# Kernel optimization log

Measured on AMD Instinct MI355X. Metric: run time of the kernel, lower is better.

The kernel has to match this reference:

```python
import jax, jax.numpy as jnp
import numpy as np
import math

V, L, D, S, F, H, B = 32000, 6, 1024, 2048, 4096, 16, 2
DK = D // H
EPS = 1e-5


def _pos_encoding(max_len, d_model):
    pos = np.arange(max_len)[:, None].astype(np.float32)
    freq = np.exp(np.arange(0, d_model, 2).astype(np.float32) * -(math.log(10000.0) / d_model))
    pe = np.zeros((max_len, d_model), dtype=np.float32)
    pe[:, 0::2] = np.sin(pos * freq)
    pe[:, 1::2] = np.cos(pos * freq)
    return jnp.asarray(pe)


def setup_inputs() -> dict:
    key = jax.random.key(0)
    ks = jax.random.split(key, 16)
    n = lambda k, shape: (jax.random.normal(k, shape, dtype=jnp.float32) * 0.02)
    return {
        "tokens": jax.random.randint(ks[0], (B, S), 0, V, dtype=jnp.int32),
        "emb": n(ks[1], (V, D)),
        "Wq": n(ks[2], (L, D, D)), "bq": jnp.zeros((L, D)),
        "Wk": n(ks[3], (L, D, D)), "bk": jnp.zeros((L, D)),
        "Wv": n(ks[4], (L, D, D)), "bv": jnp.zeros((L, D)),
        "Wo": n(ks[5], (L, D, D)), "bo": jnp.zeros((L, D)),
        "W1": n(ks[6], (L, D, F)), "b1": jnp.zeros((L, F)),
        "W2": n(ks[7], (L, F, D)), "b2": jnp.zeros((L, D)),
        "g1": jnp.ones((L, D)), "be1": jnp.zeros((L, D)),
        "g2": jnp.ones((L, D)), "be2": jnp.zeros((L, D)),
    }


def _layernorm(x, g, b):
    mu = jnp.mean(x, axis=-1, keepdims=True)
    var = jnp.var(x, axis=-1, keepdims=True)
    return (x - mu) * jax.lax.rsqrt(var + EPS) * g + b


def _encoder(tokens, emb, Wq, bq, Wk, bk, Wv, bv, Wo, bo, W1, b1, W2, b2, g1, be1, g2, be2):
    pe = _pos_encoding(S, D)
    x = emb[tokens] * jnp.float32(math.sqrt(D)) + pe  # [B,S,D]

    def layer(x, p):
        wq, bq_, wk, bk_, wv, bv_, wo, bo_, w1, b1_, w2, b2_, g1_, be1_, g2_, be2_ = p
        q = (x @ wq + bq_).reshape(B, S, H, DK)
        k = (x @ wk + bk_).reshape(B, S, H, DK)
        v = (x @ wv + bv_).reshape(B, S, H, DK)
        scores = jnp.einsum("bqhd,bkhd->bhqk", q, k) / jnp.float32(math.sqrt(DK))
        attn = jax.nn.softmax(scores, axis=-1)
        out = jnp.einsum("bhqk,bkhd->bqhd", attn, v).reshape(B, S, D)
        out = out @ wo + bo_
        x = _layernorm(x + out, g1_, be1_)
        ff = jax.nn.relu(x @ w1 + b1_) @ w2 + b2_
        x = _layernorm(x + ff, g2_, be2_)
        return x, None

    params = (Wq, bq, Wk, bk, Wv, bv, Wo, bo, W1, b1, W2, b2, g1, be1, g2, be2)
    x, _ = jax.lax.scan(layer, x, params)
    return x


def reference(tokens, emb, Wq, bq, Wk, bk, Wv, bv, Wo, bo, W1, b1, W2, b2, g1, be1, g2, be2):
    return _encoder(tokens, emb, Wq, bq, Wk, bk, Wv, bv, Wo, bo, W1, b1, W2, b2, g1, be1, g2, be2)
```

## Files before the change

kernel.cpp:

```cpp
#include <hip/hip_runtime.h>
#include <hip/hip_bf16.h>

#define DEV static __device__ __forceinline__

typedef __attribute__((ext_vector_type(8))) short bf16x8;
typedef __attribute__((ext_vector_type(4))) float f32x4;
typedef __attribute__((ext_vector_type(4))) unsigned short u16x4;
typedef __attribute__((ext_vector_type(4))) unsigned int u32x4;

constexpr int Lc = 6, Dc = 1024, Sc = 2048, Fc = 4096, Hc = 16, Bc = 2;
constexpr int Mc = Bc * Sc;
constexpr int QKVN = 3 * Dc;
constexpr float QSCALE = 0.18033688011112042f;

DEV float bf2f(unsigned short u) {
  unsigned int x = ((unsigned int)u) << 16; float f;
  __builtin_memcpy(&f, &x, 4); return f;
}
DEV unsigned short f2bf(float f) {
  unsigned int x; __builtin_memcpy(&x, &f, 4);
  x += 0x7fffu + ((x >> 16) & 1u);
  return (unsigned short)(x >> 16);
}
DEV unsigned int cvt_pk_bf16(float lo, float hi) {
  unsigned int r;
  asm("v_cvt_pk_bf16_f32 %0, %1, %2" : "=v"(r) : "v"(lo), "v"(hi));
  return r;
}

typedef __attribute__((address_space(1))) unsigned int* gas_t;
typedef __attribute__((address_space(3))) unsigned int* las_t;
DEV void gload16(const void* g, void* l) {
  __builtin_amdgcn_global_load_lds((gas_t)g, (las_t)l, 16, 0, 0);
}

DEV int vperm(int k) {
  return ((k >> 5) << 5) + (((k >> 2) & 3) << 3) + (((k >> 4) & 1) << 2) + (k & 3);
}

DEV void tr32(const float* __restrict__ W, unsigned short* __restrict__ Wt,
              int Kd, int Nd, float scale, int bx, int by, int tid,
              float (*tile)[33])
{
  const int n0 = bx * 32, k0 = by * 32;
  const int tx = tid & 31, ty = tid >> 5;
#pragma unroll
  for (int i = 0; i < 4; ++i) {
    int k = ty + i * 8;
    tile[k][tx] = W[(size_t)(k0 + k) * Nd + n0 + tx];
  }
  __syncthreads();
#pragma unroll
  for (int i = 0; i < 4; ++i) {
    int n = ty + i * 8;
    Wt[(size_t)(n0 + n) * Kd + k0 + tx] = f2bf(tile[tx][n] * scale);
  }
}

__global__ __launch_bounds__(256) void prep_weights(
    const float* __restrict__ Wq, const float* __restrict__ Wk,
    const float* __restrict__ Wv, const float* __restrict__ Wo,
    const float* __restrict__ W1, const float* __restrict__ W2,
    const float* __restrict__ bq, const float* __restrict__ bk,
    const float* __restrict__ bv,
    unsigned short* __restrict__ Wqkvt, unsigned short* __restrict__ Wot,
    unsigned short* __restrict__ W1t, unsigned short* __restrict__ W2t,
    float* __restrict__ bqkv)
{
  __shared__ float tile[32][33];
  const int id = blockIdx.x, t = threadIdx.x;
  if (id < 4096) {
    int which = id >> 10, lo = id & 1023;
    int bx = lo & 31, by = lo >> 5;
    if (which == 0)      tr32(Wq, Wqkvt, Dc, Dc, QSCALE, bx, by, t, tile);
    else if (which == 1) tr32(Wk, Wqkvt + (size_t)Dc * Dc, Dc, Dc, 1.0f, bx, by, t, tile);
    else if (which == 2) tr32(Wv, Wqkvt + (size_t)2 * Dc * Dc, Dc, Dc, 1.0f, bx, by, t, tile);
    else                 tr32(Wo, Wot, Dc, Dc, 1.0f, bx, by, t, tile);
  } else if (id < 8192) {
    int lo = id - 4096;
    tr32(W1, W1t, Dc, Fc, 1.0f, lo & 127, lo >> 7, t, tile);
  } else if (id < 12288) {
    int lo = id - 8192;
    tr32(W2, W2t, Fc, Dc, 1.0f, lo & 31, lo >> 5, t, tile);
  } else {
    int i = (id - 12288) * 256 + t;
    bqkv[i] = (i < Dc) ? bq[i] * QSCALE : (i < 2 * Dc ? bk[i - Dc] : bv[i - 2 * Dc]);
  }
}

__global__ __launch_bounds__(256) void embed_kernel(
    const int* __restrict__ tokens, const float* __restrict__ emb,
    float* __restrict__ xf, unsigned short* __restrict__ xb)
{
  const int bs = blockIdx.x;
  const int s = bs & (Sc - 1);
  const int tok = tokens[bs];
  const int d0 = threadIdx.x * 4;
  f32x4 e4 = *(const f32x4*)(emb + (size_t)tok * Dc + d0);
  f32x4 vf; u16x4 vb;
#pragma unroll
  for (int j = 0; j < 4; ++j) {
    int d = d0 + j;
    float e = e4[j] * 32.0f;
    float fr = expf((float)(d & ~1) * (-9.210340371976184f / 1024.0f));
    float arg = (float)s * fr;
    float pe = (d & 1) ? cosf(arg) : sinf(arg);
    float v = e + pe;
    vf[j] = v; vb[j] = f2bf(v);
  }
  *(f32x4*)(xf + (size_t)bs * Dc + d0) = vf;
  *(u16x4*)(xb + (size_t)bs * Dc + d0) = vb;
}

DEV void gemm256_core(const unsigned short* __restrict__ A,
                      const unsigned short* __restrict__ Bt,
                      unsigned short (*As)[256 * 64], unsigned short (*Bs)[256 * 64],
                      f32x4 (*acc)[4], int mTile, int nTile,
                      int Kstride, int k0, int nT, int t)
{
  const int lane = t & 63;
  const int g = lane >> 4, li = lane & 15;
  const int w = t >> 6;
  const int wm = w >> 2, wn = w & 3;
  const int trow = t >> 3, tslot = t & 7;
  const int asl = tslot ^ (trow & 7);
  int aoff[4];
#pragma unroll
  for (int q = 0; q < 4; ++q) {
    int R = (trow < 32) ? (q * 32 + trow) : (96 + q * 32 + trow);
    aoff[q] = (mTile + R) * Kstride + k0 + asl * 8;
  }
  int boff[4], bld[4];
#pragma unroll
  for (int k2 = 0; k2 < 4; ++k2) {
    int idx = k2 * 512 + t;
    int br = idx >> 3;
    int bs = (idx & 7) ^ (br & 7);
    boff[k2] = (nTile + br) * Kstride + k0 + bs * 8;
    bld[k2] = idx * 8;
  }

  auto stB = [&](int nb, int kt, int ph) {
    gload16(Bt + boff[ph * 2 + 0] + kt, &Bs[nb][bld[ph * 2 + 0]]);
    gload16(Bt + boff[ph * 2 + 1] + kt, &Bs[nb][bld[ph * 2 + 1]]);
  };
  auto stA = [&](int nb, int kt, int ph) {
    gload16(A + aoff[ph * 2 + 0] + kt, &As[nb][(ph * 2 + 0) * 4096 + t * 8]);
    gload16(A + aoff[ph * 2 + 1] + kt, &As[nb][(ph * 2 + 1) * 4096 + t * 8]);
  };

  stB(0, 0, 0); stB(0, 0, 1); stA(0, 0, 0); stA(0, 0, 1);
  asm volatile("s_waitcnt vmcnt(0)" ::: "memory");
  __builtin_amdgcn_s_barrier();

  int cur = 0;
  for (int tt = 0; tt < nT; ++tt) {
    const char* Ac = (const char*)As[cur];
    const char* Bc = (const char*)Bs[cur];
    const int nb = cur ^ 1;
    const int ktn = (tt + 1) << 6;
    const bool more = tt + 1 < nT;

    bf16x8 bfr[4][2];
#pragma unroll
    for (int ni = 0; ni < 4; ++ni) {
      const int rn = wn * 64 + ni * 16 + li;
#pragma unroll
      for (int ks = 0; ks < 2; ++ks) {
        const int kb = ks * 64 + (g << 4);
        bfr[ni][ks] = *(const bf16x8*)(Bc + rn * 128 + (kb ^ ((rn & 7) << 4)));
      }
    }

#pragma unroll
    for (int ph = 0; ph < 4; ++ph) {
      bf16x8 afr[2][2];
#pragma unroll
      for (int mi2 = 0; mi2 < 2; ++mi2) {
        const int rr = wm * 32 + mi2 * 16 + li;
#pragma unroll
        for (int ks = 0; ks < 2; ++ks) {
          const int kb = ks * 64 + (g << 4);
          afr[mi2][ks] = *(const bf16x8*)(Ac + ph * 8192 + rr * 128 + (kb ^ ((rr & 7) << 4)));
        }
      }
      if (more) {
        if (ph == 0)      stB(nb, ktn, 0);
        else if (ph == 1) stB(nb, ktn, 1);
        else if (ph == 2) stA(nb, ktn, 0);
        else              stA(nb, ktn, 1);
      }
      __builtin_amdgcn_s_barrier();
      __builtin_amdgcn_s_setprio(1);
#pragma unroll
      for (int mi2 = 0; mi2 < 2; ++mi2)
#pragma unroll
        for (int ni = 0; ni < 4; ++ni)
#pragma unroll
          for (int ks = 0; ks < 2; ++ks)
            acc[ph * 2 + mi2][ni] = __builtin_amdgcn_mfma_f32_16x16x32_bf16(
                afr[mi2][ks], bfr[ni][ks], acc[ph * 2 + mi2][ni], 0, 0, 0);
      __builtin_amdgcn_s_setprio(0);
      if (ph == 0)      asm volatile("s_waitcnt vmcnt(4)" ::: "memory");
      else if (ph == 1) asm volatile("s_waitcnt vmcnt(5)" ::: "memory");
      else if (ph == 2) asm volatile("s_waitcnt vmcnt(6)" ::: "memory");
      else              asm volatile("s_waitcnt vmcnt(3)" ::: "memory");
      __builtin_amdgcn_s_barrier();
    }
    cur ^= 1;
  }
}

__global__ __launch_bounds__(512) void gemm256(
    const unsigned short* __restrict__ A, const unsigned short* __restrict__ Bt,
    const float* __restrict__ bias, unsigned short* __restrict__ outB,
    unsigned short* __restrict__ Vt, int gx, int Ndim, int Kdim, int relu)
{
  __shared__ alignas(16) unsigned short As[2][256 * 64];
  __shared__ alignas(16) unsigned short Bs[2][256 * 64];
  const int t = threadIdx.x;
  const int lane = t & 63, w = t >> 6;
  const int wm = w >> 2, wn = w & 3;
  const int g = lane >> 4, li = lane & 15;
  const int nwg = gridDim.x, flat = blockIdx.x;
  const int swz = (flat & 7) * (nwg >> 3) + (flat >> 3);
  const int mTile = (swz / gx) * 256;
  const int nTile = (swz % gx) * 256;

  f32x4 acc[8][4] = {};
  gemm256_core(A, Bt, As, Bs, acc, mTile, nTile, Kdim, 0, Kdim >> 6, t);

  const bool vblk = (Vt != nullptr) && (nTile >= 2 * Dc);
#pragma unroll
  for (int mi = 0; mi < 8; ++mi) {
#pragma unroll
    for (int ni = 0; ni < 4; ++ni) {
      const int c = nTile + wn * 64 + ni * 16 + li;
      const float bvv = bias[c];
      if (!vblk) {
#pragma unroll
        for (int j = 0; j < 4; ++j) {
          const int r = mTile + wm * 128 + mi * 16 + g * 4 + j;
          float v = acc[mi][ni][j] + bvv;
          if (relu) v = fmaxf(v, 0.0f);
          outB[(size_t)r * Ndim + c] = f2bf(v);
        }
      } else {
        const int r0 = mTile + wm * 128 + mi * 16 + g * 4;
        const int b = r0 >> 11, s0 = r0 & 2047;
        const int sp = (s0 & ~63) + vperm(s0 & 63);
        u16x4 ov;
#pragma unroll
        for (int j = 0; j < 4; ++j) ov[j] = f2bf(acc[mi][ni][j] + bvv);
        *(u16x4*)(Vt + ((size_t)(b * Dc + (c - 2 * Dc))) * Sc + sp) = ov;
      }
    }
  }
}

template<int SPLIT>
__global__ __launch_bounds__(512) void gemm256_sk(
    const unsigned short* __restrict__ A, const unsigned short* __restrict__ Bt,
    unsigned short* __restrict__ part, int gx, int gy, int Ndim, int Ktot)
{
  __shared__ alignas(16) unsigned short As[2][256 * 64];
  __shared__ alignas(16) unsigned short Bs[2][256 * 64];
  const int t = threadIdx.x;
  const int lane = t & 63, w = t >> 6;
  const int wm = w >> 2, wn = w & 3;
  const int g = lane >> 4, li = lane & 15;
  const int nwg = gridDim.x, flat = blockIdx.x;
  const int swz = (flat & 7) * (nwg >> 3) + (flat >> 3);
  const int nTile = (swz % gx) * 256;
  const int mTile = ((swz / gx) % gy) * 256;
  const int z = swz / (gx * gy);
  const int Kseg = Ktot / SPLIT;

  f32x4 acc[8][4] = {};
  gemm256_core(A, Bt, As, Bs, acc, mTile, nTile, Ktot, z * Kseg, Kseg >> 6, t);

  unsigned short* po = part + (size_t)z * Mc * Ndim;
#pragma unroll
  for (int mi = 0; mi < 8; ++mi)
#pragma unroll
    for (int ni = 0; ni < 4; ++ni) {
      const int c = nTile + wn * 64 + ni * 16 + li;
#pragma unroll
      for (int j = 0; j < 4; ++j) {
        const int r = mTile + wm * 128 + mi * 16 + g * 4 + j;
        po[(size_t)r * Ndim + c] = f2bf(acc[mi][ni][j]);
      }
    }
}

__global__ __launch_bounds__(256) void attn128(
    const unsigned short* __restrict__ QKV, const unsigned short* __restrict__ Vt,
    unsigned short* __restrict__ O)
{
  __shared__ alignas(16) unsigned short Qs[128 * 64];
  __shared__ alignas(16) unsigned short Ks[2][64 * 64];
  __shared__ alignas(16) unsigned short Vs[2][64 * 64];

  const int t = threadIdx.x;
  const int lane = t & 63, w = t >> 6;
  const int g = lane >> 4, li = lane & 15;
  const int flat = blockIdx.x;
  const int idx = ((flat & 7) << 6) | (flat >> 3);
  const int qb = idx & 15, bh = idx >> 4;
  const int b = bh >> 4, h = bh & 15;

  const size_t qbase  = ((size_t)(b * Sc + qb * 128)) * QKVN + h * 64;
  const size_t kbase0 = ((size_t)b * Sc) * QKVN + Dc + h * 64;
  const size_t vbase0 = ((size_t)(b * Dc + h * 64)) * Sc;

#pragma unroll
  for (int i = 0; i < 4; ++i) {
    int idx2 = i * 256 + t, row = idx2 >> 3, sl = (idx2 & 7) ^ (row & 7);
    gload16(QKV + qbase + (size_t)row * QKVN + sl * 8, &Qs[idx2 * 8]);
  }
  const unsigned short* kg[2];
  const unsigned short* vg[2];
  int loff[2];
#pragma unroll
  for (int i = 0; i < 2; ++i) {
    int idx2 = i * 256 + t, row = idx2 >> 3, sl = (idx2 & 7) ^ (row & 7);
    kg[i] = QKV + kbase0 + (size_t)row * QKVN + sl * 8;
    vg[i] = Vt + vbase0 + (size_t)row * Sc + sl * 8;
    loff[i] = idx2 * 8;
  }
  gload16(kg[0], &Ks[0][loff[0]]); gload16(kg[1], &Ks[0][loff[1]]);
  gload16(vg[0], &Vs[0][loff[0]]); gload16(vg[1], &Vs[0][loff[1]]);
  kg[0] += 64 * QKVN; kg[1] += 64 * QKVN;
  vg[0] += 64;        vg[1] += 64;
  __syncthreads();

  bf16x8 qf[2][2];
#pragma unroll
  for (int qi = 0; qi < 2; ++qi) {
    const int rq = w * 32 + qi * 16 + li;
#pragma unroll
    for (int ks = 0; ks < 2; ++ks) {
      const int kb = ks * 64 + (g << 4);
      qf[qi][ks] = *(const bf16x8*)((const char*)Qs + rq * 128 + (kb ^ ((rq & 7) << 4)));
    }
  }
  bf16x8 ones;
#pragma unroll
  for (int e = 0; e < 8; ++e) ones[e] = (short)0x3F80;

  f32x4 acc_o[2][4] = {};
  f32x4 acc_l[2] = {};
  int cur = 0;

  for (int kc = 0; kc < Sc; kc += 64) {
    if (kc + 64 < Sc) {
      const int nxt = cur ^ 1;
      gload16(kg[0], &Ks[nxt][loff[0]]); gload16(kg[1], &Ks[nxt][loff[1]]);
      gload16(vg[0], &Vs[nxt][loff[0]]); gload16(vg[1], &Vs[nxt][loff[1]]);
      kg[0] += 64 * QKVN; kg[1] += 64 * QKVN;
      vg[0] += 64;        vg[1] += 64;
    }

    f32x4 accs[2][4] = {};
#pragma unroll
    for (int ks = 0; ks < 2; ++ks) {
      const int kb = ks * 64 + (g << 4);
#pragma unroll
      for (int ni = 0; ni < 4; ++ni) {
        int rk = ni * 16 + li;
        bf16x8 ak = *(const bf16x8*)((const char*)Ks[cur] + rk * 128 + (kb ^ ((rk & 7) << 4)));
        accs[0][ni] = __builtin_amdgcn_mfma_f32_16x16x32_bf16(ak, qf[0][ks], accs[0][ni], 0, 0, 0);
        accs[1][ni] = __builtin_amdgcn_mfma_f32_16x16x32_bf16(ak, qf[1][ks], accs[1][ni], 0, 0, 0);
      }
    }

    unsigned int pk[2][4][2];
#pragma unroll
    for (int qi = 0; qi < 2; ++qi)
#pragma unroll
      for (int ni = 0; ni < 4; ++ni) {
        float p0 = exp2f(accs[qi][ni][0]);
        float p1 = exp2f(accs[qi][ni][1]);
        float p2 = exp2f(accs[qi][ni][2]);
        float p3 = exp2f(accs[qi][ni][3]);
        pk[qi][ni][0] = cvt_pk_bf16(p0, p1);
        pk[qi][ni][1] = cvt_pk_bf16(p2, p3);
      }

#pragma unroll
    for (int ks = 0; ks < 2; ++ks) {
      bf16x8 ap[2];
#pragma unroll
      for (int qi = 0; qi < 2; ++qi) {
        u32x4 av = {pk[qi][2 * ks][0], pk[qi][2 * ks][1],
                    pk[qi][2 * ks + 1][0], pk[qi][2 * ks + 1][1]};
        ap[qi] = __builtin_bit_cast(bf16x8, av);
        acc_l[qi] = __builtin_amdgcn_mfma_f32_16x16x32_bf16(ap[qi], ones, acc_l[qi], 0, 0, 0);
      }
      const int kb = ks * 64 + (g << 4);
#pragma unroll
      for (int ni = 0; ni < 4; ++ni) {
        int rd = ni * 16 + li;
        bf16x8 bv = *(const bf16x8*)((const char*)Vs[cur] + rd * 128 + (kb ^ ((rd & 7) << 4)));
        acc_o[0][ni] = __builtin_amdgcn_mfma_f32_16x16x32_bf16(ap[0], bv, acc_o[0][ni], 0, 0, 0);
        acc_o[1][ni] = __builtin_amdgcn_mfma_f32_16x16x32_bf16(ap[1], bv, acc_o[1][ni], 0, 0, 0);
      }
    }

    __syncthreads();
    cur ^= 1;
  }

  const size_t obase = ((size_t)(b * Sc + qb * 128)) * Dc + h * 64;
#pragma unroll
  for (int qi = 0; qi < 2; ++qi) {
    float denom[4];
#pragma unroll
    for (int j = 0; j < 4; ++j) denom[j] = 1.0f / acc_l[qi][j];
#pragma unroll
    for (int ni = 0; ni < 4; ++ni)
#pragma unroll
      for (int j = 0; j < 4; ++j) {
        int q = w * 32 + qi * 16 + g * 4 + j;
        O[obase + (size_t)q * Dc + ni * 16 + li] = f2bf(acc_o[qi][ni][j] * denom[j]);
      }
  }
}

template<int SPLIT>
__global__ __launch_bounds__(256) void reduce_ln(
    const unsigned short* __restrict__ part, const float* __restrict__ bias,
    const float* __restrict__ res, const float* __restrict__ g,
    const float* __restrict__ be, float* __restrict__ xf_out,
    unsigned short* __restrict__ xb_out)
{
  const int row = blockIdx.x, t = threadIdx.x;
  const size_t off = (size_t)row * Dc + t * 4;
  f32x4 v = *(const f32x4*)(res + off);
  v += *(const f32x4*)(bias + t * 4);
#pragma unroll
  for (int s = 0; s < SPLIT; ++s) {
    u16x4 pv = *(const u16x4*)(part + (size_t)s * Mc * Dc + off);
#pragma unroll
    for (int j = 0; j < 4; ++j) v[j] += bf2f(pv[j]);
  }

  float sm = v[0] + v[1] + v[2] + v[3];
  float q = v[0]*v[0] + v[1]*v[1] + v[2]*v[2] + v[3]*v[3];
#pragma unroll
  for (int o = 32; o; o >>= 1) {
    sm += __shfl_down(sm, o);
    q += __shfl_down(q, o);
  }
  __shared__ float rs_[4], rq_[4];
  const int lane = t & 63, w = t >> 6;
  if (lane == 0) { rs_[w] = sm; rq_[w] = q; }
  __syncthreads();
  sm = rs_[0] + rs_[1] + rs_[2] + rs_[3];
  q = rq_[0] + rq_[1] + rq_[2] + rq_[3];
  const float mu = sm * (1.0f / 1024.0f);
  const float var = q * (1.0f / 1024.0f) - mu * mu;
  const float rstd = rsqrtf(var + 1e-5f);
  f32x4 vg = *(const f32x4*)(g + t * 4);
  f32x4 vb = *(const f32x4*)(be + t * 4);
  f32x4 o; u16x4 ob;
#pragma unroll
  for (int j = 0; j < 4; ++j) {
    float val = (v[j] - mu) * rstd * vg[j] + vb[j];
    o[j] = val; ob[j] = f2bf(val);
  }
  *(f32x4*)(xf_out + off) = o;
  *(u16x4*)(xb_out + off) = ob;
}

extern "C" void kernel_launch(void* const* d_in, const int* in_sizes, int n_in,
                              void* d_out, int out_size, void* d_ws, size_t ws_size,
                              hipStream_t stream)
{
  (void)in_sizes; (void)n_in; (void)out_size; (void)ws_size;
  const int*   tokens = (const int*)d_in[0];
  const float* emb = (const float*)d_in[1];
  const float* Wq = (const float*)d_in[2];
  const float* bq = (const float*)d_in[3];
  const float* Wk = (const float*)d_in[4];
  const float* bk = (const float*)d_in[5];
  const float* Wv = (const float*)d_in[6];
  const float* bv = (const float*)d_in[7];
  const float* Wo = (const float*)d_in[8];
  const float* bo = (const float*)d_in[9];
  const float* W1 = (const float*)d_in[10];
  const float* b1 = (const float*)d_in[11];
  const float* W2 = (const float*)d_in[12];
  const float* b2 = (const float*)d_in[13];
  const float* g1 = (const float*)d_in[14];
  const float* be1 = (const float*)d_in[15];
  const float* g2 = (const float*)d_in[16];
  const float* be2 = (const float*)d_in[17];

  char* p = (char*)d_ws;
  auto take = [&](size_t bytes) { char* q = p; p += bytes; return q; };
  unsigned short* Wqkvt = (unsigned short*)take((size_t)3 * Dc * Dc * 2);
  unsigned short* Wot = (unsigned short*)take((size_t)Dc * Dc * 2);
  unsigned short* W1t = (unsigned short*)take((size_t)Dc * Fc * 2);
  unsigned short* W2t = (unsigned short*)take((size_t)Fc * Dc * 2);
  float*          bqkv = (float*)take((size_t)QKVN * 4);
  float*          xf  = (float*)take((size_t)Mc * Dc * 4);
  unsigned short* xb  = (unsigned short*)take((size_t)Mc * Dc * 2);
  unsigned short* QKVb = (unsigned short*)take((size_t)Mc * QKVN * 2);
  unsigned short* Vtb = (unsigned short*)take((size_t)Bc * Dc * Sc * 2);
  unsigned short* Ob  = (unsigned short*)take((size_t)Mc * Dc * 2);
  unsigned short* ff1 = (unsigned short*)take((size_t)Mc * Fc * 2);
  unsigned short* part = QKVb;

  dim3 blk(256);
  embed_kernel<<<dim3(Mc), blk, 0, stream>>>(tokens, emb, xf, xb);

  for (int l = 0; l < Lc; ++l) {
    const size_t owD = (size_t)l * Dc * Dc;
    const size_t owF = (size_t)l * Dc * Fc;
    const int ob = l * Dc;
    prep_weights<<<dim3(12300), blk, 0, stream>>>(
        Wq + owD, Wk + owD, Wv + owD, Wo + owD, W1 + owF, W2 + owF,
        bq + ob, bk + ob, bv + ob, Wqkvt, Wot, W1t, W2t, bqkv);

    gemm256<<<dim3((Mc / 256) * (QKVN / 256)), dim3(512), 0, stream>>>(
        xb, Wqkvt, bqkv, QKVb, Vtb, QKVN / 256, QKVN, Dc, 0);
    attn128<<<dim3(512), blk, 0, stream>>>(QKVb, Vtb, Ob);

    gemm256_sk<4><<<dim3((Dc / 256) * (Mc / 256) * 4), dim3(512), 0, stream>>>(
        Ob, Wot, part, Dc / 256, Mc / 256, Dc, Dc);
    reduce_ln<4><<<dim3(Mc), blk, 0, stream>>>(
        part, bo + ob, xf, g1 + ob, be1 + ob, xf, xb);

    gemm256<<<dim3((Mc / 256) * (Fc / 256)), dim3(512), 0, stream>>>(
        xb, W1t, b1 + l * Fc, ff1, nullptr, Fc / 256, Fc, Dc, 1);

    gemm256_sk<4><<<dim3((Dc / 256) * (Mc / 256) * 4), dim3(512), 0, stream>>>(
        ff1, W2t, part, Dc / 256, Mc / 256, Dc, Fc);
    reduce_ln<4><<<dim3(Mc), blk, 0, stream>>>(
        part, b2 + ob, xf, g2 + ob, be2 + ob,
        (l == Lc - 1) ? (float*)d_out : xf, xb);
  }
}
```

Baseline: 1.430 ms.

## Batch weight prep for all layers in one launch and enlarge attention query tile

Weight transposition and bf16 conversion for all six layers now run in a single up-front launch into per-layer workspace buffers, replacing six separate per-layer prep launches. The attention kernel now processes 256 queries per block instead of 128, so each block reuses every loaded K/V tile across twice as many MFMAs. The aim is to cut launch overhead and halve K/V global and LDS traffic per query. In exchange the workspace grows, the attention grid drops to 256 blocks, and per-thread register pressure roughly doubles, which may lower occupancy.

```diff
diff --git a/kernel.cpp b/kernel.cpp
--- a/kernel.cpp
+++ b/kernel.cpp
@@ -68,23 +68,33 @@
     float* __restrict__ bqkv)
 {
   __shared__ float tile[32][33];
-  const int id = blockIdx.x, t = threadIdx.x;
+  const int l = blockIdx.x / 12300;
+  const int id = blockIdx.x % 12300;
+  const int t = threadIdx.x;
+  const size_t owD = (size_t)l * Dc * Dc, owF = (size_t)l * Dc * Fc;
+  unsigned short* Wqkvt_l = Wqkvt + (size_t)l * 3 * Dc * Dc;
+  unsigned short* Wot_l = Wot + (size_t)l * Dc * Dc;
+  unsigned short* W1t_l = W1t + owF;
+  unsigned short* W2t_l = W2t + owF;
   if (id < 4096) {
     int which = id >> 10, lo = id & 1023;
     int bx = lo & 31, by = lo >> 5;
-    if (which == 0)      tr32(Wq, Wqkvt, Dc, Dc, QSCALE, bx, by, t, tile);
-    else if (which == 1) tr32(Wk, Wqkvt + (size_t)Dc * Dc, Dc, Dc, 1.0f, bx, by, t, tile);
-    else if (which == 2) tr32(Wv, Wqkvt + (size_t)2 * Dc * Dc, Dc, Dc, 1.0f, bx, by, t, tile);
-    else                 tr32(Wo, Wot, Dc, Dc, 1.0f, bx, by, t, tile);
+    if (which == 0)      tr32(Wq + owD, Wqkvt_l, Dc, Dc, QSCALE, bx, by, t, tile);
+    else if (which == 1) tr32(Wk + owD, Wqkvt_l + (size_t)Dc * Dc, Dc, Dc, 1.0f, bx, by, t, tile);
+    else if (which == 2) tr32(Wv + owD, Wqkvt_l + (size_t)2 * Dc * Dc, Dc, Dc, 1.0f, bx, by, t, tile);
+    else                 tr32(Wo + owD, Wot_l, Dc, Dc, 1.0f, bx, by, t, tile);
   } else if (id < 8192) {
     int lo = id - 4096;
-    tr32(W1, W1t, Dc, Fc, 1.0f, lo & 127, lo >> 7, t, tile);
+    tr32(W1 + owF, W1t_l, Dc, Fc, 1.0f, lo & 127, lo >> 7, t, tile);
   } else if (id < 12288) {
     int lo = id - 8192;
-    tr32(W2, W2t, Fc, Dc, 1.0f, lo & 31, lo >> 5, t, tile);
+    tr32(W2 + owF, W2t_l, Fc, Dc, 1.0f, lo & 31, lo >> 5, t, tile);
   } else {
     int i = (id - 12288) * 256 + t;
-    bqkv[i] = (i < Dc) ? bq[i] * QSCALE : (i < 2 * Dc ? bk[i - Dc] : bv[i - 2 * Dc]);
+    const int ob = l * Dc;
+    bqkv[l * QKVN + i] =
+        (i < Dc) ? bq[ob + i] * QSCALE
+                 : (i < 2 * Dc ? bk[ob + i - Dc] : bv[ob + i - 2 * Dc]);
   }
 }
 
@@ -293,11 +303,11 @@
     }
 }
 
-__global__ __launch_bounds__(256) void attn128(
+__global__ __launch_bounds__(256) void attn256(
     const unsigned short* __restrict__ QKV, const unsigned short* __restrict__ Vt,
     unsigned short* __restrict__ O)
 {
-  __shared__ alignas(16) unsigned short Qs[128 * 64];
+  __shared__ alignas(16) unsigned short Qs[256 * 64];
   __shared__ alignas(16) unsigned short Ks[2][64 * 64];
   __shared__ alignas(16) unsigned short Vs[2][64 * 64];
 
@@ -305,16 +315,16 @@
   const int lane = t & 63, w = t >> 6;
   const int g = lane >> 4, li = lane & 15;
   const int flat = blockIdx.x;
-  const int idx = ((flat & 7) << 6) | (flat >> 3);
-  const int qb = idx & 15, bh = idx >> 4;
+  const int idx = ((flat & 7) << 5) | (flat >> 3);
+  const int qb = idx & 7, bh = idx >> 3;
   const int b = bh >> 4, h = bh & 15;
 
-  const size_t qbase  = ((size_t)(b * Sc + qb * 128)) * QKVN + h * 64;
+  const size_t qbase  = ((size_t)(b * Sc + qb * 256)) * QKVN + h * 64;
   const size_t kbase0 = ((size_t)b * Sc) * QKVN + Dc + h * 64;
   const size_t vbase0 = ((size_t)(b * Dc + h * 64)) * Sc;
 
 #pragma unroll
-  for (int i = 0; i < 4; ++i) {
+  for (int i = 0; i < 8; ++i) {
     int idx2 = i * 256 + t, row = idx2 >> 3, sl = (idx2 & 7) ^ (row & 7);
     gload16(QKV + qbase + (size_t)row * QKVN + sl * 8, &Qs[idx2 * 8]);
   }
@@ -334,10 +344,10 @@
   vg[0] += 64;        vg[1] += 64;
   __syncthreads();
 
-  bf16x8 qf[2][2];
-#pragma unroll
-  for (int qi = 0; qi < 2; ++qi) {
-    const int rq = w * 32 + qi * 16 + li;
+  bf16x8 qf[4][2];
+#pragma unroll
+  for (int qi = 0; qi < 4; ++qi) {
+    const int rq = w * 64 + qi * 16 + li;
 #pragma unroll
     for (int ks = 0; ks < 2; ++ks) {
       const int kb = ks * 64 + (g << 4);
@@ -348,8 +358,8 @@
 #pragma unroll
   for (int e = 0; e < 8; ++e) ones[e] = (short)0x3F80;
 
-  f32x4 acc_o[2][4] = {};
-  f32x4 acc_l[2] = {};
+  f32x4 acc_o[4][4] = {};
+  f32x4 acc_l[4] = {};
   int cur = 0;
 
   for (int kc = 0; kc < Sc; kc += 64) {
@@ -361,7 +371,7 @@
       vg[0] += 64;        vg[1] += 64;
     }
 
-    f32x4 accs[2][4] = {};
+    f32x4 accs[4][4] = {};
 #pragma unroll
     for (int ks = 0; ks < 2; ++ks) {
       const int kb = ks * 64 + (g << 4);
@@ -369,14 +379,16 @@
       for (int ni = 0; ni < 4; ++ni) {
         int rk = ni * 16 + li;
         bf16x8 ak = *(const bf16x8*)((const char*)Ks[cur] + rk * 128 + (kb ^ ((rk & 7) << 4)));
-        accs[0][ni] = __builtin_amdgcn_mfma_f32_16x16x32_bf16(ak, qf[0][ks], accs[0][ni], 0, 0, 0);
-        accs[1][ni] = __builtin_amdgcn_mfma_f32_16x16x32_bf16(ak, qf[1][ks], accs[1][ni], 0, 0, 0);
-      }
-    }
-
-    unsigned int pk[2][4][2];
-#pragma unroll
-    for (int qi = 0; qi < 2; ++qi)
+#pragma unroll
+        for (int qi = 0; qi < 4; ++qi)
+          accs[qi][ni] = __builtin_amdgcn_mfma_f32_16x16x32_bf16(
+              ak, qf[qi][ks], accs[qi][ni], 0, 0, 0);
+      }
+    }
+
+    unsigned int pk[4][4][2];
+#pragma unroll
+    for (int qi = 0; qi < 4; ++qi)
 #pragma unroll
       for (int ni = 0; ni < 4; ++ni) {
         float p0 = exp2f(accs[qi][ni][0]);
@@ -389,9 +401,9 @@
 
 #pragma unroll
     for (int ks = 0; ks < 2; ++ks) {
-      bf16x8 ap[2];
-#pragma unroll
-      for (int qi = 0; qi < 2; ++qi) {
+      bf16x8 ap[4];
+#pragma unroll
+      for (int qi = 0; qi < 4; ++qi) {
         u32x4 av = {pk[qi][2 * ks][0], pk[qi][2 * ks][1],
                     pk[qi][2 * ks + 1][0], pk[qi][2 * ks + 1][1]};
         ap[qi] = __builtin_bit_cast(bf16x8, av);
@@ -402,8 +414,10 @@
       for (int ni = 0; ni < 4; ++ni) {
         int rd = ni * 16 + li;
         bf16x8 bv = *(const bf16x8*)((const char*)Vs[cur] + rd * 128 + (kb ^ ((rd & 7) << 4)));
-        acc_o[0][ni] = __builtin_amdgcn_mfma_f32_16x16x32_bf16(ap[0], bv, acc_o[0][ni], 0, 0, 0);
-        acc_o[1][ni] = __builtin_amdgcn_mfma_f32_16x16x32_bf16(ap[1], bv, acc_o[1][ni], 0, 0, 0);
+#pragma unroll
+        for (int qi = 0; qi < 4; ++qi)
+          acc_o[qi][ni] = __builtin_amdgcn_mfma_f32_16x16x32_bf16(
+              ap[qi], bv, acc_o[qi][ni], 0, 0, 0);
       }
     }
 
@@ -411,9 +425,9 @@
     cur ^= 1;
   }
 
-  const size_t obase = ((size_t)(b * Sc + qb * 128)) * Dc + h * 64;
-#pragma unroll
-  for (int qi = 0; qi < 2; ++qi) {
+  const size_t obase = ((size_t)(b * Sc + qb * 256)) * Dc + h * 64;
+#pragma unroll
+  for (int qi = 0; qi < 4; ++qi) {
     float denom[4];
 #pragma unroll
     for (int j = 0; j < 4; ++j) denom[j] = 1.0f / acc_l[qi][j];
@@ -421,7 +435,7 @@
     for (int ni = 0; ni < 4; ++ni)
 #pragma unroll
       for (int j = 0; j < 4; ++j) {
-        int q = w * 32 + qi * 16 + g * 4 + j;
+        int q = w * 64 + qi * 16 + g * 4 + j;
         O[obase + (size_t)q * Dc + ni * 16 + li] = f2bf(acc_o[qi][ni][j] * denom[j]);
       }
   }
@@ -499,11 +513,11 @@
 
   char* p = (char*)d_ws;
   auto take = [&](size_t bytes) { char* q = p; p += bytes; return q; };
-  unsigned short* Wqkvt = (unsigned short*)take((size_t)3 * Dc * Dc * 2);
-  unsigned short* Wot = (unsigned short*)take((size_t)Dc * Dc * 2);
-  unsigned short* W1t = (unsigned short*)take((size_t)Dc * Fc * 2);
-  unsigned short* W2t = (unsigned short*)take((size_t)Fc * Dc * 2);
-  float*          bqkv = (float*)take((size_t)QKVN * 4);
+  unsigned short* Wqkvt = (unsigned short*)take((size_t)Lc * 3 * Dc * Dc * 2);
+  unsigned short* Wot = (unsigned short*)take((size_t)Lc * Dc * Dc * 2);
+  unsigned short* W1t = (unsigned short*)take((size_t)Lc * Dc * Fc * 2);
+  unsigned short* W2t = (unsigned short*)take((size_t)Lc * Fc * Dc * 2);
+  float*          bqkv = (float*)take((size_t)Lc * QKVN * 4);
   float*          xf  = (float*)take((size_t)Mc * Dc * 4);
   unsigned short* xb  = (unsigned short*)take((size_t)Mc * Dc * 2);
   unsigned short* QKVb = (unsigned short*)take((size_t)Mc * QKVN * 2);
@@ -513,30 +527,31 @@
   unsigned short* part = QKVb;
 
   dim3 blk(256);
+  prep_weights<<<dim3(Lc * 12300), blk, 0, stream>>>(
+      Wq, Wk, Wv, Wo, W1, W2, bq, bk, bv, Wqkvt, Wot, W1t, W2t, bqkv);
   embed_kernel<<<dim3(Mc), blk, 0, stream>>>(tokens, emb, xf, xb);
 
   for (int l = 0; l < Lc; ++l) {
-    const size_t owD = (size_t)l * Dc * Dc;
-    const size_t owF = (size_t)l * Dc * Fc;
     const int ob = l * Dc;
-    prep_weights<<<dim3(12300), blk, 0, stream>>>(
-        Wq + owD, Wk + owD, Wv + owD, Wo + owD, W1 + owF, W2 + owF,
-        bq + ob, bk + ob, bv + ob, Wqkvt, Wot, W1t, W2t, bqkv);
+    const unsigned short* Wqkvt_l = Wqkvt + (size_t)l * 3 * Dc * Dc;
+    const unsigned short* Wot_l = Wot + (size_t)l * Dc * Dc;
+    const unsigned short* W1t_l = W1t + (size_t)l * Dc * Fc;
+    const unsigned short* W2t_l = W2t + (size_t)l * Fc * Dc;
 
     gemm256<<<dim3((Mc / 256) * (QKVN / 256)), dim3(512), 0, stream>>>(
-        xb, Wqkvt, bqkv, QKVb, Vtb, QKVN / 256, QKVN, Dc, 0);
-    attn128<<<dim3(512), blk, 0, stream>>>(QKVb, Vtb, Ob);
+        xb, Wqkvt_l, bqkv + l * QKVN, QKVb, Vtb, QKVN / 256, QKVN, Dc, 0);
+    attn256<<<dim3(256), blk, 0, stream>>>(QKVb, Vtb, Ob);
 
     gemm256_sk<4><<<dim3((Dc / 256) * (Mc / 256) * 4), dim3(512), 0, stream>>>(
-        Ob, Wot, part, Dc / 256, Mc / 256, Dc, Dc);
+        Ob, Wot_l, part, Dc / 256, Mc / 256, Dc, Dc);
     reduce_ln<4><<<dim3(Mc), blk, 0, stream>>>(
         part, bo + ob, xf, g1 + ob, be1 + ob, xf, xb);
 
     gemm256<<<dim3((Mc / 256) * (Fc / 256)), dim3(512), 0, stream>>>(
-        xb, W1t, b1 + l * Fc, ff1, nullptr, Fc / 256, Fc, Dc, 1);
+        xb, W1t_l, b1 + l * Fc, ff1, nullptr, Fc / 256, Fc, Dc, 1);
 
     gemm256_sk<4><<<dim3((Dc / 256) * (Mc / 256) * 4), dim3(512), 0, stream>>>(
-        ff1, W2t, part, Dc / 256, Mc / 256, Dc, Fc);
+        ff1, W2t_l, part, Dc / 256, Mc / 256, Dc, Fc);
     reduce_ln<4><<<dim3(Mc), blk, 0, stream>>>(
         part, b2 + ob, xf, g2 + ob, be2 + ob,
         (l == Lc - 1) ? (float*)d_out : xf, xb);
```

Measured after the change: 1.505 ms. 1.05x slower.
